# Optimization experiments

Hardware: AMD Instinct MI355X
Metric: run time of the kernel (lower is better)

Reference implementation:

```python
import jax, jax.numpy as jnp
from jax import lax
import numpy as np

NB_HEAD = 8
D_MODEL = 64
KERNEL = 3


def setup_inputs() -> dict:
    key = jax.random.key(0)
    k1, k2, k3, k4, k5 = jax.random.split(key, 5)
    B, N, T, D = 16, 1024, 24, D_MODEL
    value = jax.random.normal(k1, (B, N, T, D), dtype=jnp.float32)
    # Conv2d(d_model, d_model, (1, kernel_size)) weights (OIHW) + bias
    fan_in = D * 1 * KERNEL
    bound = 1.0 / np.sqrt(fan_in)
    W_conv = jax.random.uniform(k2, (D, D, 1, KERNEL), jnp.float32, -bound, bound)
    b_conv = jax.random.uniform(k3, (D,), jnp.float32, -bound, bound)
    # Linear(d_model, d_model): W (out, in), bias (out,)
    lb = 1.0 / np.sqrt(D)
    W_lin = jax.random.uniform(k4, (D, D), jnp.float32, -lb, lb)
    b_lin = jax.random.uniform(k5, (D,), jnp.float32, -lb, lb)
    return {"value": value, "W_conv": W_conv, "b_conv": b_conv,
            "W_lin": W_lin, "b_lin": b_lin}


def reference(value, W_conv, b_conv, W_lin, b_lin):
    B, N, T, D = value.shape
    h = NB_HEAD
    d_k = D // h
    pad = (KERNEL - 1) // 2
    # conv1D_aware_temporal_context1 on value.permute(0,3,1,2): (B, D, N, T)
    x = jnp.transpose(value, (0, 3, 1, 2))
    x = lax.conv_general_dilated(
        x, W_conv, window_strides=(1, 1), padding=[(0, 0), (pad, pad)],
        dimension_numbers=("NCHW", "OIHW", "NCHW"))
    x = x + b_conv[None, :, None, None]
    # view(B, h, d_k, N, T).permute(0,3,1,4,2) -> (B, N, h, T, d_k)
    v = jnp.transpose(x.reshape(B, h, d_k, N, T), (0, 3, 1, 4, 2))
    # relation_matrix_h is the tridiagonal all-ones band -> out[t] = v[t-1]+v[t]+v[t+1]
    vp = jnp.pad(v, ((0, 0), (0, 0), (0, 0), (1, 1), (0, 0)))
    v = vp[..., :-2, :] + vp[..., 1:-1, :] + vp[..., 2:, :]
    # transpose(2,3) then merge heads: (B, N, T, h*d_k)
    v = jnp.transpose(v, (0, 1, 3, 2, 4)).reshape(B, N, T, h * d_k)
    # linear_output1 + relu
    out = jax.nn.relu(jnp.einsum("bntd,od->bnto", v, W_lin) + b_lin)
    return out
```

## Files before the change

kernel.cpp:

```cpp
#include <hip/hip_runtime.h>
#include <hip/hip_bf16.h>


typedef __attribute__((ext_vector_type(8))) short short8;
typedef __attribute__((ext_vector_type(8))) __bf16 bf16x8;
typedef __attribute__((ext_vector_type(4))) float f4;

#define ROWS_PB 2
#define VP_STRIDE 72
#define ROW_SHORTS (26 * VP_STRIDE)
#define WREG_SHORTS (ROWS_PB * ROW_SHORTS)

__device__ __forceinline__ unsigned short f2bfu(float f) {
    return __bfloat16_as_ushort(__float2bfloat16(f));
}

__global__ void prep_kernel(const float* __restrict__ Wconv,
                            const float* __restrict__ bconv,
                            const float* __restrict__ Wlin,
                            const float* __restrict__ blin,
                            __hip_bfloat16* __restrict__ wbig,
                            float* __restrict__ biasC,
                            float* __restrict__ blinF) {
    __shared__ float Wl[4096];
    const int tid = threadIdx.x;
    for (int c = tid; c < 4096; c += 256) Wl[c] = Wlin[c];
    __syncthreads();
    int idx = blockIdx.x * 256 + tid;
    if (idx < 64 * 192) {
        int o = idx / 192;
        int j = idx - o * 192;
        int k = j >> 6;
        int i = j & 63;
        float acc = 0.0f;
        for (int c = 0; c < 64; ++c)
            acc += Wl[o * 64 + c] * Wconv[c * 192 + i * 3 + k];
        wbig[o * 192 + j] = __float2bfloat16(acc);
    } else if (idx < 64 * 192 + 64) {
        int o = idx - 64 * 192;
        float acc = 0.0f;
        for (int c = 0; c < 64; ++c)
            acc += Wl[o * 64 + c] * bconv[c];
        biasC[o] = acc;
    } else if (idx < 64 * 192 + 128) {
        int o = idx - (64 * 192 + 64);
        blinF[o] = blin[o];
    }
}

__global__ __launch_bounds__(256, 4) void fused_kernel(
    const float* __restrict__ value,
    const __hip_bfloat16* __restrict__ wbig,
    const float* __restrict__ biasC,
    const float* __restrict__ blinF,
    float* __restrict__ out) {
    __shared__ __align__(16) short Vlds[4 * WREG_SHORTS];

    const int tid = threadIdx.x;
    const int wave = tid >> 6;
    const int lane = tid & 63;
    const int lane15 = lane & 15;
    const int quad = lane >> 4;
    const long base_row = (long)blockIdx.x * ROWS_PB;

    short* const wbase = Vlds + wave * WREG_SHORTS;

    f4 pre[12];
    const int tq = quad;
    const int d4 = lane15 << 2;
    {
        const float* vb = value + base_row * 1536 + tq * 64 + d4;
        #pragma unroll
        for (int rr = 0; rr < 2; ++rr)
            #pragma unroll
            for (int j = 0; j < 6; ++j)
                pre[rr * 6 + j] = *(const f4*)(vb + rr * 1536 + j * 256);
    }

    const short* wsrc = (const short*)wbig;
    const int k0 = quad * 8;
    bf16x8 breg[6];
    #pragma unroll
    for (int ks = 0; ks < 6; ++ks)
        breg[ks] = __builtin_bit_cast(bf16x8,
            *(const short8*)(wsrc + (wave * 16 + lane15) * 192 + ks * 32 + k0));

    const int o = wave * 16 + lane15;
    const float bc = biasC[o];
    const float bl = blinF[o];

    if (lane < 32) {
        int rr = (lane >> 4) & 1;
        int which = (lane >> 3) & 1;
        int d8 = (lane & 7) << 3;
        uint4 z; z.x = 0; z.y = 0; z.z = 0; z.w = 0;
        *(uint4*)(wbase + rr * ROW_SHORTS + which * (25 * VP_STRIDE) + d8) = z;
    }
    {
        short* lbase = wbase + (tq + 1) * VP_STRIDE + d4;
        #pragma unroll
        for (int rr = 0; rr < 2; ++rr)
            #pragma unroll
            for (int j = 0; j < 6; ++j) {
                f4 p = pre[rr * 6 + j];
                ushort4 u;
                u.x = f2bfu(p.x); u.y = f2bfu(p.y);
                u.z = f2bfu(p.z); u.w = f2bfu(p.w);
                *(ushort4*)(lbase + rr * ROW_SHORTS + j * (4 * VP_STRIDE)) = u;
            }
    }

    int aoff[3];
    #pragma unroll
    for (int mt = 0; mt < 3; ++mt) {
        int m = mt * 16 + lane15;
        int rr = m / 24;
        int s = m - rr * 24;
        aoff[mt] = rr * ROW_SHORTS + s * VP_STRIDE;
    }
    f4 acc[3];
    #pragma unroll
    for (int mt = 0; mt < 3; ++mt) {
        f4 zz = {0.f, 0.f, 0.f, 0.f};
        acc[mt] = zz;
    }
    #pragma unroll
    for (int ks = 0; ks < 6; ++ks) {
        int k = ks * 32 + k0;
        int ka = ((k >> 6) * VP_STRIDE) + (k & 63);
        #pragma unroll
        for (int mt = 0; mt < 3; ++mt) {
            bf16x8 a = __builtin_bit_cast(bf16x8,
                *(const short8*)(wbase + aoff[mt] + ka));
            acc[mt] = __builtin_amdgcn_mfma_f32_16x16x32_bf16(
                a, breg[ks], acc[mt], 0, 0, 0);
        }
    }

    const float b3 = 3.0f * bc + bl;
    const float b2 = 2.0f * bc + bl;
    const int srcP = (lane + 48) & 63;
    const int srcN = (lane + 16) & 63;
    float* pbase = out + (long)blockIdx.x * 3072 + quad * 256 + o;
    #pragma unroll
    for (int mt = 0; mt < 3; ++mt) {
        const int mtp = (mt > 0) ? mt - 1 : 0;
        const int mtn = (mt < 2) ? mt + 1 : 2;
        float sendP = (quad == 3) ? acc[mtp][3] : acc[mt][3];
        float sendN = (quad == 0) ? acc[mtn][0] : acc[mt][0];
        float prev0 = __shfl(sendP, srcP, 64);
        float next3 = __shfl(sendN, srcN, 64);
        const bool t0  = (mt == 0) ? (quad == 0)
                       : ((mt == 1) ? (quad == 2) : false);
        const bool t23 = (mt == 2) ? (quad == 3)
                       : ((mt == 1) ? (quad == 1) : false);
        float s0 = acc[mt][0] + acc[mt][1] + (t0  ? b2 : (prev0 + b3));
        float s1 = acc[mt][0] + acc[mt][1] + acc[mt][2] + b3;
        float s2 = acc[mt][1] + acc[mt][2] + acc[mt][3] + b3;
        float s3 = acc[mt][2] + acc[mt][3] + (t23 ? b2 : (next3 + b3));
        float* p = pbase + mt * 1024;
        p[0]   = fmaxf(s0, 0.0f);
        p[64]  = fmaxf(s1, 0.0f);
        p[128] = fmaxf(s2, 0.0f);
        p[192] = fmaxf(s3, 0.0f);
    }
}

extern "C" void kernel_launch(void* const* d_in, const int* in_sizes, int n_in,
                              void* d_out, int out_size, void* d_ws, size_t ws_size,
                              hipStream_t stream) {
    const float* value = (const float*)d_in[0];
    const float* Wconv = (const float*)d_in[1];
    const float* bconv = (const float*)d_in[2];
    const float* Wlin  = (const float*)d_in[3];
    const float* blin  = (const float*)d_in[4];
    float* out = (float*)d_out;

    __hip_bfloat16* wbig = (__hip_bfloat16*)d_ws;
    float* biasC = (float*)((char*)d_ws + 24576);
    float* blinF = (float*)((char*)d_ws + 24832);

    prep_kernel<<<49, 256, 0, stream>>>(Wconv, bconv, Wlin, blin, wbig, biasC, blinF);
    fused_kernel<<<8192, 256, 0, stream>>>(value, wbig, biasC, blinF, out);
}
```

Before: 200.3 us.

## Load MFMA A-operands directly from global memory, removing LDS staging

```diff
diff --git a/kernel.cpp b/kernel.cpp
--- a/kernel.cpp
+++ b/kernel.cpp
@@ -3,13 +3,11 @@
 
 
 typedef __attribute__((ext_vector_type(8))) short short8;
+typedef __attribute__((ext_vector_type(8))) unsigned short ushort8;
 typedef __attribute__((ext_vector_type(8))) __bf16 bf16x8;
 typedef __attribute__((ext_vector_type(4))) float f4;
 
 #define ROWS_PB 2
-#define VP_STRIDE 72
-#define ROW_SHORTS (26 * VP_STRIDE)
-#define WREG_SHORTS (ROWS_PB * ROW_SHORTS)
 
 __device__ __forceinline__ unsigned short f2bfu(float f) {
     return __bfloat16_as_ushort(__float2bfloat16(f));
@@ -48,14 +46,12 @@
     }
 }
 
-__global__ __launch_bounds__(256, 4) void fused_kernel(
+__global__ __launch_bounds__(256, 3) void fused_kernel(
     const float* __restrict__ value,
     const __hip_bfloat16* __restrict__ wbig,
     const float* __restrict__ biasC,
     const float* __restrict__ blinF,
     float* __restrict__ out) {
-    __shared__ __align__(16) short Vlds[4 * WREG_SHORTS];
-
     const int tid = threadIdx.x;
     const int wave = tid >> 6;
     const int lane = tid & 63;
@@ -63,77 +59,62 @@
     const int quad = lane >> 4;
     const long base_row = (long)blockIdx.x * ROWS_PB;
 
-    short* const wbase = Vlds + wave * WREG_SHORTS;
-
-    f4 pre[12];
-    const int tq = quad;
-    const int d4 = lane15 << 2;
-    {
-        const float* vb = value + base_row * 1536 + tq * 64 + d4;
-        #pragma unroll
-        for (int rr = 0; rr < 2; ++rr)
-            #pragma unroll
-            for (int j = 0; j < 6; ++j)
-                pre[rr * 6 + j] = *(const f4*)(vb + rr * 1536 + j * 256);
-    }
-
     const short* wsrc = (const short*)wbig;
-    const int k0 = quad * 8;
     bf16x8 breg[6];
     #pragma unroll
     for (int ks = 0; ks < 6; ++ks)
         breg[ks] = __builtin_bit_cast(bf16x8,
-            *(const short8*)(wsrc + (wave * 16 + lane15) * 192 + ks * 32 + k0));
+            *(const short8*)(wsrc + (wave * 16 + lane15) * 192
+                             + ks * 32 + quad * 8));
 
     const int o = wave * 16 + lane15;
     const float bc = biasC[o];
     const float bl = blinF[o];
 
-    if (lane < 32) {
-        int rr = (lane >> 4) & 1;
-        int which = (lane >> 3) & 1;
-        int d8 = (lane & 7) << 3;
-        uint4 z; z.x = 0; z.y = 0; z.z = 0; z.w = 0;
-        *(uint4*)(wbase + rr * ROW_SHORTS + which * (25 * VP_STRIDE) + d8) = z;
-    }
-    {
-        short* lbase = wbase + (tq + 1) * VP_STRIDE + d4;
-        #pragma unroll
-        for (int rr = 0; rr < 2; ++rr)
-            #pragma unroll
-            for (int j = 0; j < 6; ++j) {
-                f4 p = pre[rr * 6 + j];
-                ushort4 u;
-                u.x = f2bfu(p.x); u.y = f2bfu(p.y);
-                u.z = f2bfu(p.z); u.w = f2bfu(p.w);
-                *(ushort4*)(lbase + rr * ROW_SHORTS + j * (4 * VP_STRIDE)) = u;
-            }
-    }
+    const float* vb = value + base_row * 1536 + quad * 8;
 
-    int aoff[3];
-    #pragma unroll
-    for (int mt = 0; mt < 3; ++mt) {
-        int m = mt * 16 + lane15;
-        int rr = m / 24;
-        int s = m - rr * 24;
-        aoff[mt] = rr * ROW_SHORTS + s * VP_STRIDE;
-    }
     f4 acc[3];
     #pragma unroll
     for (int mt = 0; mt < 3; ++mt) {
         f4 zz = {0.f, 0.f, 0.f, 0.f};
         acc[mt] = zz;
     }
+
     #pragma unroll
-    for (int ks = 0; ks < 6; ++ks) {
-        int k = ks * 32 + k0;
-        int ka = ((k >> 6) * VP_STRIDE) + (k & 63);
+    for (int mt = 0; mt < 3; ++mt) {
+        const int m = mt * 16 + lane15;
+        const int rr = (m >= 24) ? 1 : 0;
+        const int s = m - rr * 24;
+        const bool lo = (s == 0);
+        const bool hi = (s == 23);
+        const float* rbase = vb + rr * 1536;
+        const float* r0 = rbase + (lo ? 0 : (s - 1)) * 64;
+        const float* r1 = rbase + s * 64;
+        const float* r2 = rbase + (hi ? 23 : (s + 1)) * 64;
+
+        f4 p[12];
+        p[0]  = *(const f4*)(r0);       p[1]  = *(const f4*)(r0 + 4);
+        p[2]  = *(const f4*)(r0 + 32);  p[3]  = *(const f4*)(r0 + 36);
+        p[4]  = *(const f4*)(r1);       p[5]  = *(const f4*)(r1 + 4);
+        p[6]  = *(const f4*)(r1 + 32);  p[7]  = *(const f4*)(r1 + 36);
+        p[8]  = *(const f4*)(r2);       p[9]  = *(const f4*)(r2 + 4);
+        p[10] = *(const f4*)(r2 + 32);  p[11] = *(const f4*)(r2 + 36);
+
+        f4 zf = {0.f, 0.f, 0.f, 0.f};
+        if (lo) { p[0] = zf; p[1] = zf; p[2] = zf; p[3] = zf; }
+        if (hi) { p[8] = zf; p[9] = zf; p[10] = zf; p[11] = zf; }
+
         #pragma unroll
-        for (int mt = 0; mt < 3; ++mt) {
-            bf16x8 a = __builtin_bit_cast(bf16x8,
-                *(const short8*)(wbase + aoff[mt] + ka));
+        for (int ks = 0; ks < 6; ++ks) {
+            f4 plo = p[ks * 2];
+            f4 phi = p[ks * 2 + 1];
+            ushort8 u;
+            u[0] = f2bfu(plo.x); u[1] = f2bfu(plo.y);
+            u[2] = f2bfu(plo.z); u[3] = f2bfu(plo.w);
+            u[4] = f2bfu(phi.x); u[5] = f2bfu(phi.y);
+            u[6] = f2bfu(phi.z); u[7] = f2bfu(phi.w);
             acc[mt] = __builtin_amdgcn_mfma_f32_16x16x32_bf16(
-                a, breg[ks], acc[mt], 0, 0, 0);
+                __builtin_bit_cast(bf16x8, u), breg[ks], acc[mt], 0, 0, 0);
         }
     }
 
```

New measurement: 292.1 us. +45.8%, slower.
